# Performance work log

Hardware: AMD Instinct MI355X
Metric: run time of the kernel (lower is better)

## Reference

```python
import jax, jax.numpy as jnp
import numpy as np

# Constants from the torch module
S_DECAY = 0.95    # sentence_decay
P_DECAY = 0.99    # paragraph_decay
D_DECAY = 0.999   # document_decay
ALPHA = 0.1       # delta_update alpha for sentence/paragraph
DOC_ALPHA = 0.05  # delta_update alpha for document
BETA = 1.0
PARA_GROUP = 5    # sentences per paragraph
EPS = 1e-12       # F.normalize eps


def _normalize(x):
    # matches torch.nn.functional.normalize(x, dim=-1)
    return x / jnp.maximum(jnp.linalg.norm(x, axis=-1, keepdims=True), EPS)


def _delta_step(M, kn, v, alpha, beta):
    # M: [H, dk, dv]; kn: [dk] (already L2-normalized); v: [dv]
    # M_new = M @ (I - alpha * kn kn^T) + beta * kn v^T   (erase matrix is symmetric,
    # so the einsum 'hkv,hkj->hjv' form equals this rank-1 update -- no dk x dk matrix needed)
    kTM = jnp.einsum('k,hkv->hv', kn, M)                       # [H, dv]
    return M - alpha * kn[None, :, None] * kTM[:, None, :] \
             + beta * (kn[:, None] * v[None, :])[None, :, :]


def _scan_updates(M0, K, V, decay, alpha, beta):
    # Streaming delta-rule: per step, decay then erase/write.
    def step(M, kv):
        k, v = kv
        M = M * decay
        M = _delta_step(M, _normalize(k), v, alpha, beta)
        return M, None
    M, _ = jax.lax.scan(step, M0, (K, V))
    return M


def setup_inputs() -> dict:
    key = jax.random.key(0)
    ks = jax.random.split(key, 7)
    T, d_emb, d_k, d_v, H = 1000, 768, 256, 256, 8
    emb = jax.random.normal(ks[0], (T, d_emb), dtype=jnp.float32)
    q = jax.random.normal(ks[1], (d_k,), dtype=jnp.float32)
    W_k = jax.random.normal(ks[2], (d_emb, d_k), dtype=jnp.float32) * 0.02
    b_k = jax.random.normal(ks[3], (d_k,), dtype=jnp.float32) * 0.02
    W_v = jax.random.normal(ks[4], (d_emb, d_v), dtype=jnp.float32) * 0.02
    b_v = jax.random.normal(ks[5], (d_v,), dtype=jnp.float32) * 0.02
    M_sent0 = jnp.zeros((H, d_k, d_v), dtype=jnp.float32)
    M_para0 = jnp.zeros((H, d_k, d_v), dtype=jnp.float32)
    M_doc0 = jnp.zeros((H, d_k, d_v), dtype=jnp.float32)
    return {"emb": emb, "q": q, "W_k": W_k, "b_k": b_k, "W_v": W_v, "b_v": b_v,
            "M_sent0": M_sent0, "M_para0": M_para0, "M_doc0": M_doc0}


def reference(emb, q, W_k, b_k, W_v, b_v, M_sent0, M_para0, M_doc0):
    T, d_emb = emb.shape
    # Level 1: sentence memory -- one delta update per sentence embedding
    K = emb @ W_k + b_k            # [T, dk]
    V = emb @ W_v + b_v            # [T, dv]
    M_sent = _scan_updates(M_sent0, K, V, S_DECAY, ALPHA, BETA)
    # Level 2: paragraph memory -- mean of each group of 5 sentence embeddings
    para_emb = emb.reshape(T // PARA_GROUP, PARA_GROUP, d_emb).mean(axis=1)
    PK = para_emb @ W_k + b_k
    PV = para_emb @ W_v + b_v
    M_para = _scan_updates(M_para0, PK, PV, P_DECAY, ALPHA, BETA)
    # Level 3: document memory -- single update from paragraph-memory statistics
    doc_k = M_para.mean(axis=0).mean(axis=-1)   # [dk]
    doc_v = M_para.mean(axis=0).mean(axis=0)    # [dv]
    M_doc = M_doc0 * D_DECAY
    M_doc = _delta_step(M_doc, _normalize(doc_k), doc_v, DOC_ALPHA, BETA)
    # recall(q, level='all')
    qn = _normalize(q)
    def recall(M):
        return jnp.einsum('hkv,k->hv', M, qn).mean(axis=0)   # [dv]
    return 0.2 * recall(M_sent) + 0.3 * recall(M_para) + 0.5 * recall(M_doc)
```

## Files before the change

### kernel.cpp

```cpp
#include <hip/hip_runtime.h>
#include <hip/hip_bf16.h>

#define ALPHA   0.1f
#define S_DECAY 0.95f
#define P_DECAY 0.99f
#define D_EMB   768
#define DK      256

template<int ctrl, int row_mask>
__device__ __forceinline__ float dpp_add(float x) {
    int y = __builtin_amdgcn_update_dpp(0, __float_as_int(x), ctrl, row_mask, 0xF, true);
    return x + __int_as_float(y);
}

template<int N>
__device__ __forceinline__ void wave_allred_arr(float (&x)[N]) {
#pragma unroll
    for (int n = 0; n < N; ++n) x[n] = dpp_add<0xB1,  0xF>(x[n]);
#pragma unroll
    for (int n = 0; n < N; ++n) x[n] = dpp_add<0x4E,  0xF>(x[n]);
#pragma unroll
    for (int n = 0; n < N; ++n) x[n] = dpp_add<0x141, 0xF>(x[n]);
#pragma unroll
    for (int n = 0; n < N; ++n) x[n] = dpp_add<0x140, 0xF>(x[n]);
#pragma unroll
    for (int n = 0; n < N; ++n) x[n] = dpp_add<0x142, 0xA>(x[n]);
#pragma unroll
    for (int n = 0; n < N; ++n) x[n] = dpp_add<0x143, 0xC>(x[n]);
#pragma unroll
    for (int n = 0; n < N; ++n)
        x[n] = __int_as_float(__builtin_amdgcn_readlane(__float_as_int(x[n]), 63));
}

__device__ __forceinline__ float dot4v(const float4& a, const float4& b) {
    float t0 = a.x * b.x; t0 = fmaf(a.y, b.y, t0);
    float t1 = a.z * b.z; t1 = fmaf(a.w, b.w, t1);
    return t0 + t1;
}

__device__ __forceinline__ float rl(float x, int lane) {
    return __int_as_float(__builtin_amdgcn_readlane(__float_as_int(x), lane));
}

__global__ __launch_bounds__(256) void prep_kernel(
    const float* __restrict__ emb,
    const float* __restrict__ Wk, const float* __restrict__ bk,
    const float* __restrict__ Wv, const float* __restrict__ bv,
    float* __restrict__ K, float* __restrict__ V, float* __restrict__ USrev,
    float* __restrict__ out, int T)
{
    const int tid = threadIdx.x;
    const int bid = blockIdx.x;
    const int NBLK = (T / 4) * 2;
    if (bid >= NBLK) {
        const int PADS = ((T + 63) / 64) * 64;
        for (int i = tid; i < (PADS - T) * DK; i += 256) USrev[(size_t)T * DK + i] = 0.f;
        out[tid] = 0.f;
        return;
    }
    const int mat = bid & 1;
    const int r0  = (bid >> 1) * 4;

    __shared__ float se[4][D_EMB];
    __shared__ float s_red[4][4];

    const float4* emb4 = reinterpret_cast<const float4*>(emb);
#pragma unroll
    for (int r = 0; r < 4; ++r) {
        if (tid < D_EMB / 4)
            reinterpret_cast<float4*>(se[r])[tid] = emb4[(size_t)(r0 + r) * (D_EMB / 4) + tid];
    }
    __syncthreads();

    const float* Wp = mat ? Wv : Wk;
    const float* bp = mat ? bv : bk;
    const int j = tid;

    float a0 = 0.f, a1 = 0.f, a2 = 0.f, a3 = 0.f;
    float c0 = Wp[j],        c1 = Wp[j + DK],     c2 = Wp[j + 2*DK], c3 = Wp[j + 3*DK];
    float p0 = Wp[j + 4*DK], p1 = Wp[j + 5*DK],   p2 = Wp[j + 6*DK], p3 = Wp[j + 7*DK];

    for (int d = 0; d < D_EMB; d += 4) {
        int dn = d + 8; if (dn >= D_EMB) dn = 0;
        const float* wn = Wp + (size_t)dn * DK + j;
        float n0 = wn[0], n1 = wn[DK], n2 = wn[2*DK], n3 = wn[3*DK];

        float4 e0 = *reinterpret_cast<const float4*>(&se[0][d]);
        float4 e1 = *reinterpret_cast<const float4*>(&se[1][d]);
        float4 e2 = *reinterpret_cast<const float4*>(&se[2][d]);
        float4 e3 = *reinterpret_cast<const float4*>(&se[3][d]);
// ... 10 lines not shown
        c0 = p0; c1 = p1; c2 = p2; c3 = p3;
        p0 = n0; p1 = n1; p2 = n2; p3 = n3;
    }

    float bj = bp[j];
    float o0 = a0 + bj, o1 = a1 + bj, o2 = a2 + bj, o3 = a3 + bj;
    float* dst = mat ? V : K;
    dst[(size_t)(r0 + 0) * DK + j] = o0;
    dst[(size_t)(r0 + 1) * DK + j] = o1;
    dst[(size_t)(r0 + 2) * DK + j] = o2;
    dst[(size_t)(r0 + 3) * DK + j] = o3;

    if (mat == 0) {
        const int wave = tid >> 6, l = tid & 63;
        float red[4] = { o0*o0, o1*o1, o2*o2, o3*o3 };
        wave_allred_arr(red);
        if (l == 0) {
            s_red[wave][0] = red[0]; s_red[wave][1] = red[1];
            s_red[wave][2] = red[2]; s_red[wave][3] = red[3];
        }
        __syncthreads();
        float t0 = s_red[0][0] + s_red[1][0] + s_red[2][0] + s_red[3][0];
        float t1 = s_red[0][1] + s_red[1][1] + s_red[2][1] + s_red[3][1];
        float t2 = s_red[0][2] + s_red[1][2] + s_red[2][2] + s_red[3][2];
        float t3 = s_red[0][3] + s_red[1][3] + s_red[2][3] + s_red[3][3];
        USrev[(size_t)(T - 1 - (r0 + 0)) * DK + j] = o0 * (1.0f / fmaxf(sqrtf(t0), 1e-12f));
        USrev[(size_t)(T - 1 - (r0 + 1)) * DK + j] = o1 * (1.0f / fmaxf(sqrtf(t1), 1e-12f));
        USrev[(size_t)(T - 1 - (r0 + 2)) * DK + j] = o2 * (1.0f / fmaxf(sqrtf(t2), 1e-12f));
        USrev[(size_t)(T - 1 - (r0 + 3)) * DK + j] = o3 * (1.0f / fmaxf(sqrtf(t3), 1e-12f));
    }
}

#define SU_STRIDE 260
__global__ __launch_bounds__(512) void mid_kernel(
    const float* __restrict__ K, const float* __restrict__ V,
    const float* __restrict__ USrev,
    float* __restrict__ UPrev, float* __restrict__ UPfwd,
    float* __restrict__ PV, float* __restrict__ SVv,
    float* __restrict__ AinvT, float* __restrict__ F1, float* __restrict__ biasF,
    int P, int NCS, int NCP)
{
    __shared__ __align__(16) float sU[64 * SU_STRIDE];
    __shared__ __align__(16) float sA[64 * 65];
    __shared__ float s_pd[64];
    __shared__ float s_sv[64];
    __shared__ float4 s_f1w[4][64];
    float* sX = sU;

    const int tid = threadIdx.x, wv = tid >> 6, l = tid & 63;
    const int bid = blockIdx.x;
    int type, m;
    if (bid < NCS)            { type = 0; m = bid; }
    else if (bid < NCS + NCP) { type = 1; m = bid - NCS; }
    else                      { type = 2; m = bid - NCS - NCP; }

    if (type == 2) {
        if (tid < 64) s_pd[tid] = powf(P_DECAY, (float)tid);
        __syncthreads();
    }

    if (type == 0) {
        const float4* U4 = reinterpret_cast<const float4*>(USrev) + (size_t)m * 4096;
        for (int idx = tid; idx < 4096; idx += 512) {
            float4 t = U4[idx];
            int row = idx >> 6, c4 = (idx & 63) << 2;
            *reinterpret_cast<float4*>(&sU[row * SU_STRIDE + c4]) = t;
        }
    } else if (type == 1) {
        if (tid < 256) {
            const float4* K4 = reinterpret_cast<const float4*>(K);
            for (int ii = 0; ii < 16; ii += 2) {
                const int iA = wv * 16 + ii, iB = iA + 1;
                const int pA = P - 1 - (64 * m + iA);
                const int pB = P - 1 - (64 * m + iB);
                float4 ka[5], kb[5];
                if (pA >= 0) {
#pragma unroll
                    for (int s = 0; s < 5; ++s) ka[s] = K4[(size_t)(5 * pA + s) * 64 + l];
                }
                if (pB >= 0) {
#pragma unroll
                    for (int s = 0; s < 5; ++s) kb[s] = K4[(size_t)(5 * pB + s) * 64 + l];
                }
// ... 172 lines not shown
        float x[16];
#pragma unroll
        for (int r = 0; r < 16; ++r) x[r] = (base + r == l && wv < 4) ? 1.f : 0.f;
        for (int s = 0; s < 4; ++s) {
            if (wv == s) {
#pragma unroll
                for (int i = 1; i < 16; ++i)
#pragma unroll
                    for (int jj = 0; jj < 16; ++jj)
                        if (jj < i)
                            x[i] = fmaf(-sA[(base + i) * 65 + (base + jj)], x[jj], x[i]);
#pragma unroll
                for (int r = 0; r < 16; ++r) sX[(base + r) * 65 + l] = x[r];
            }
            __syncthreads();
            if (wv > s && wv < 4) {
#pragma unroll
                for (int i = 0; i < 16; ++i) {
                    float xi = sX[(s * 16 + i) * 65 + l];
#pragma unroll
                    for (int r = 0; r < 16; ++r)
                        x[r] = fmaf(-sA[(base + r) * 65 + (s * 16 + i)], xi, x[r]);
                }
            }
        }
    }
    __syncthreads();

    float* dstA = AinvT + (size_t)bid * 4096;
    for (int idx = tid; idx < 4096; idx += 512) {
        int jcol = idx >> 6, irow = idx & 63;
        dstA[idx] = sX[irow * 65 + jcol];
    }
}

__global__ __launch_bounds__(512) void solve_kernel(
    const float* __restrict__ USrev, const float* __restrict__ UPrev,
    const float* __restrict__ UPfwd, const float* __restrict__ AinvT,
    const float* __restrict__ F1, const float* __restrict__ biasF,
    const float* __restrict__ q,
    float* __restrict__ BS, float* __restrict__ BPB1, float* __restrict__ BPB2,
    float* __restrict__ gscal, int NCS, int NCP)
{
    __shared__ float s_cp[8][64], s_cp2[8][64];
    __shared__ float4 s_part[8][64], s_part2[8][64];
    __shared__ float s_powd[65];
    const int tid = threadIdx.x, wave = tid >> 6, l = tid & 63;
    const int wb = wave * 8;
    if (tid <= 64) s_powd[tid] = powf(P_DECAY, (float)tid);

    float4 q4 = reinterpret_cast<const float4*>(q)[l];
    float qs[1] = { dot4v(q4, q4) };
    wave_allred_arr(qs);
    float qinv = 1.0f / fmaxf(sqrtf(qs[0]), 1e-12f);
    float4 qn = make_float4(q4.x * qinv, q4.y * qinv, q4.z * qinv, q4.w * qinv);
    __syncthreads();

    if (blockIdx.x == 0) {
        float4 w1 = qn;
        const float4* U4 = reinterpret_cast<const float4*>(USrev);
        float4 curU[8]; float curX[8];
#pragma unroll
        for (int r = 0; r < 8; ++r) {
            curU[r] = U4[(size_t)(wb + r) * 64 + l];
            curX[r] = AinvT[(size_t)(wb + r) * 64 + l];
        }
        for (int m = 0; m < NCS; ++m) {
            float4 nxtU[8]; float nxtX[8];
            if (m + 1 < NCS) {
#pragma unroll
                for (int r = 0; r < 8; ++r) {
                    nxtU[r] = U4[(size_t)(m + 1) * 4096 + (size_t)(wb + r) * 64 + l];
                    nxtX[r] = AinvT[(size_t)(m + 1) * 4096 + (size_t)(wb + r) * 64 + l];
                }
            }
            float d[8];
#pragma unroll
            for (int r = 0; r < 8; ++r) d[r] = dot4v(curU[r], w1);
            wave_allred_arr(d);
            if (l == 0) {
#pragma unroll
                for (int r = 0; r < 8; ++r) BS[m * 64 + wb + r] = d[r];
            }
            float cp = 0.f;
#pragma unroll
            for (int r = 0; r < 8; ++r) cp = fmaf(curX[r], d[r], cp);
            s_cp[wave][l] = cp;
            __syncthreads();
            float cl = 0.f;
#pragma unroll
            for (int w = 0; w < 8; ++w) cl += s_cp[w][l];
            float4 part = make_float4(0.f, 0.f, 0.f, 0.f);
#pragma unroll
            for (int r = 0; r < 8; ++r) {
                float ci = rl(cl, wb + r);
                part.x = fmaf(ci, curU[r].x, part.x); part.y = fmaf(ci, curU[r].y, part.y);
                part.z = fmaf(ci, curU[r].z, part.z); part.w = fmaf(ci, curU[r].w, part.w);
            }
            s_part[wave][l] = part;
            __syncthreads();
            float4 s = make_float4(0.f, 0.f, 0.f, 0.f);
#pragma unroll
            for (int w = 0; w < 8; ++w) {
                float4 p = s_part[w][l];
                s.x += p.x; s.y += p.y; s.z += p.z; s.w += p.w;
            }
            w1.x = fmaf(-ALPHA, s.x, w1.x); w1.y = fmaf(-ALPHA, s.y, w1.y);
            w1.z = fmaf(-ALPHA, s.z, w1.z); w1.w = fmaf(-ALPHA, s.w, w1.w);
            if (m + 1 < NCS) {
#pragma unroll
                for (int r = 0; r < 8; ++r) { curU[r] = nxtU[r]; curX[r] = nxtX[r]; }
            }
        }
    } else {
        {
            float4 w1 = qn;
            float4 w2 = make_float4(1.f, 1.f, 1.f, 1.f);
            const float4* U4 = reinterpret_cast<const float4*>(UPrev);
            float4 curU[8]; float curX[8];
#pragma unroll
            for (int r = 0; r < 8; ++r) {
                curU[r] = U4[(size_t)(wb + r) * 64 + l];
                curX[r] = AinvT[(size_t)NCS * 4096 + (size_t)(wb + r) * 64 + l];
            }
            for (int m = 0; m < NCP; ++m) {
                float4 nxtU[8]; float nxtX[8];
                if (m + 1 < NCP) {
#pragma unroll
                    for (int r = 0; r < 8; ++r) {
                        nxtU[r] = U4[(size_t)(m + 1) * 4096 + (size_t)(wb + r) * 64 + l];
                        nxtX[r] = AinvT[(size_t)(NCS + m + 1) * 4096 + (size_t)(wb + r) * 64 + l];
                    }
                }
                float d[16];
#pragma unroll
                for (int r = 0; r < 8; ++r) {
                    d[r]     = dot4v(curU[r], w1);
                    d[8 + r] = dot4v(curU[r], w2);
                }
                wave_allred_arr(d);
                if (l == 0) {
#pragma unroll
                    for (int r = 0; r < 8; ++r) {
                        BPB1[m * 64 + wb + r] = d[r];
                        BPB2[m * 64 + wb + r] = d[8 + r];
                    }
                }
                float cp1 = 0.f, cp2 = 0.f;
#pragma unroll
                for (int r = 0; r < 8; ++r) {
                    cp1 = fmaf(curX[r], d[r], cp1);
                    cp2 = fmaf(curX[r], d[8 + r], cp2);
                }
                s_cp[wave][l] = cp1; s_cp2[wave][l] = cp2;
                __syncthreads();
                float cl1 = 0.f, cl2 = 0.f;
#pragma unroll
                for (int w = 0; w < 8; ++w) { cl1 += s_cp[w][l]; cl2 += s_cp2[w][l]; }
                float4 p1 = make_float4(0.f,0.f,0.f,0.f), p2 = make_float4(0.f,0.f,0.f,0.f);
#pragma unroll
                for (int r = 0; r < 8; ++r) {
                    float c1 = rl(cl1, wb + r), c2 = rl(cl2, wb + r);
                    p1.x = fmaf(c1, curU[r].x, p1.x); p1.y = fmaf(c1, curU[r].y, p1.y);
                    p1.z = fmaf(c1, curU[r].z, p1.z); p1.w = fmaf(c1, curU[r].w, p1.w);
                    p2.x = fmaf(c2, curU[r].x, p2.x); p2.y = fmaf(c2, curU[r].y, p2.y);
                    p2.z = fmaf(c2, curU[r].z, p2.z); p2.w = fmaf(c2, curU[r].w, p2.w);
                }
                s_part[wave][l] = p1; s_part2[wave][l] = p2;
                __syncthreads();
                float4 s1 = make_float4(0.f,0.f,0.f,0.f), s2 = make_float4(0.f,0.f,0.f,0.f);
#pragma unroll
                for (int w = 0; w < 8; ++w) {
                    float4 a = s_part[w][l];  float4 b = s_part2[w][l];
                    s1.x += a.x; s1.y += a.y; s1.z += a.z; s1.w += a.w;
                    s2.x += b.x; s2.y += b.y; s2.z += b.z; s2.w += b.w;
                }
                w1.x = fmaf(-ALPHA, s1.x, w1.x); w1.y = fmaf(-ALPHA, s1.y, w1.y);
                w1.z = fmaf(-ALPHA, s1.z, w1.z); w1.w = fmaf(-ALPHA, s1.w, w1.w);
                w2.x = fmaf(-ALPHA, s2.x, w2.x); w2.y = fmaf(-ALPHA, s2.y, w2.y);
                w2.z = fmaf(-ALPHA, s2.z, w2.z); w2.w = fmaf(-ALPHA, s2.w, w2.w);
                if (m + 1 < NCP) {
#pragma unroll
                    for (int r = 0; r < 8; ++r) { curU[r] = nxtU[r]; curX[r] = nxtX[r]; }
                }
            }
        }
        __syncthreads();
        float4 y = make_float4(0.f, 0.f, 0.f, 0.f);
        {
            const float4* U4 = reinterpret_cast<const float4*>(UPfwd);
            float4 curU[8]; float curX[8];
#pragma unroll
            for (int r = 0; r < 8; ++r) {
                curU[r] = U4[(size_t)(wb + r) * 64 + l];
                curX[r] = AinvT[(size_t)(NCS + NCP) * 4096 + (size_t)(wb + r) * 64 + l];
            }
            for (int m = 0; m < NCP; ++m) {
                float4 nxtU[8]; float nxtX[8];
                if (m + 1 < NCP) {
#pragma unroll
                    for (int r = 0; r < 8; ++r) {
                        nxtU[r] = U4[(size_t)(m + 1) * 4096 + (size_t)(wb + r) * 64 + l];
                        nxtX[r] = AinvT[(size_t)(NCS + NCP + m + 1) * 4096 + (size_t)(wb + r) * 64 + l];
                    }
                }
                float biasr[8];
#pragma unroll
                for (int r = 0; r < 8; ++r) biasr[r] = biasF[m * 64 + wb + r];
                float4 f1 = reinterpret_cast<const float4*>(F1)[(size_t)m * 64 + l];
                float d[8];
#pragma unroll
                for (int r = 0; r < 8; ++r) d[r] = dot4v(curU[r], y);
                wave_allred_arr(d);
#pragma unroll
                for (int r = 0; r < 8; ++r)
                    d[r] = fmaf(s_powd[wb + r + 1], d[r], biasr[r]);
                float cp = 0.f;
#pragma unroll
                for (int r = 0; r < 8; ++r) cp = fmaf(curX[r], d[r], cp);
                s_cp[wave][l] = cp;
                __syncthreads();
                float cl = 0.f;
#pragma unroll
                for (int w = 0; w < 8; ++w) cl += s_cp[w][l];
                float4 part = make_float4(0.f, 0.f, 0.f, 0.f);
#pragma unroll
                for (int r = 0; r < 8; ++r) {
                    float ci = s_powd[63 - (wb + r)] * rl(cl, wb + r);
                    part.x = fmaf(ci, curU[r].x, part.x); part.y = fmaf(ci, curU[r].y, part.y);
                    part.z = fmaf(ci, curU[r].z, part.z); part.w = fmaf(ci, curU[r].w, part.w);
                }
                s_part[wave][l] = part;
                __syncthreads();
                float4 s = make_float4(0.f, 0.f, 0.f, 0.f);
#pragma unroll
                for (int w = 0; w < 8; ++w) {
                    float4 p = s_part[w][l];
                    s.x += p.x; s.y += p.y; s.z += p.z; s.w += p.w;
                }
                float d64 = s_powd[64];
                y.x = fmaf(d64, y.x, fmaf(-ALPHA, s.x, f1.x));
                y.y = fmaf(d64, y.y, fmaf(-ALPHA, s.y, f1.y));
                y.z = fmaf(d64, y.z, fmaf(-ALPHA, s.z, f1.z));
                y.w = fmaf(d64, y.w, fmaf(-ALPHA, s.w, f1.w));
                if (m + 1 < NCP) {
#pragma unroll
                    for (int r = 0; r < 8; ++r) { curU[r] = nxtU[r]; curX[r] = nxtX[r]; }
                }
            }
        }
        float fin[2] = { dot4v(y, y), dot4v(qn, y) };
        wave_allred_arr(fin);
        if (tid == 0) gscal[0] = fin[1] / fmaxf(sqrtf(fin[0]), 2.56e-10f);
    }
}

__global__ __launch_bounds__(256) void accum_kernel(
    const float* __restrict__ V, const float* __restrict__ PV,
    const float* __restrict__ AinvT,
    const float* __restrict__ BS, const float* __restrict__ BPB1,
    const float* __restrict__ BPB2, const float* __restrict__ gscal,
    float* __restrict__ out, int T, int P, int NCS, int NCP)
{
    __shared__ float s_b[64], s_cp[4][64], wc[64];
    const int b = blockIdx.x, t = threadIdx.x;
    const float* src; const float* B; int i0, realN, chunk, ci; float decay;
    if (b < NCS)            { src = V;  B = BS;   ci = b;             realN = T; decay = S_DECAY; chunk = b; }
    else if (b < NCS + NCP) { src = PV; B = BPB1; ci = b - NCS;       realN = P; decay = P_DECAY; chunk = b; }
    else                    { src = PV; B = BPB2; ci = b - NCS - NCP; realN = P; decay = P_DECAY; chunk = b - NCP; }
    i0 = ci * 64;
    if (t < 64) s_b[t] = B[ci * 64 + t];
    __syncthreads();
    {
        const int part = t >> 6, k = t & 63;
        const float* Xc = AinvT + (size_t)chunk * 4096;
        float cp = 0.f;
#pragma unroll
        for (int jj = 0; jj < 16; ++jj) {
            int j = part * 16 + jj;
            cp = fmaf(Xc[j * 64 + k], s_b[j], cp);
        }
        s_cp[part][k] = cp;
    }
    __syncthreads();
    if (t < 64) {
        float c = s_cp[0][t] + s_cp[1][t] + s_cp[2][t] + s_cp[3][t];
        wc[t] = powf(decay, (float)(i0 + t)) * c;
    }
    __syncthreads();
    const int k = t;
    float acc = 0.f;
    for (int ii = 0; ii < 64; ++ii) {
        int i = i0 + ii;
        if (i < realN)
            acc = fmaf(wc[ii], src[(size_t)(realN - 1 - i) * DK + k], acc);
    }
    float wlev;
    if (b < NCS)            wlev = 0.2f;
    else if (b < NCS + NCP) wlev = 0.3f;
    else                    wlev = (0.5f / 256.0f) * gscal[0];
    atomicAdd(&out[k], wlev * acc);
}

extern "C" void kernel_launch(void* const* d_in, const int* in_sizes, int n_in,
                              void* d_out, int out_size, void* d_ws, size_t ws_size,
                              hipStream_t stream) {
    const float* emb = (const float*)d_in[0];
    const float* q   = (const float*)d_in[1];
    const float* Wk  = (const float*)d_in[2];
    const float* bk  = (const float*)d_in[3];
    const float* Wv  = (const float*)d_in[4];
    const float* bv  = (const float*)d_in[5];

    const int T = in_sizes[0] / D_EMB;
    const int P = T / 5;
    const int NCS  = (T + 63) / 64;
    const int NCP  = (P + 63) / 64;
    const int PADS = NCS * 64;
    const int PADP = NCP * 64;
    const int NCH  = NCS + 2 * NCP;

    float* ws    = (float*)d_ws;
    float* K     = ws;
    float* V     = K     + (size_t)T * DK;
    float* PV    = V     + (size_t)T * DK;
    float* USrev = PV    + (size_t)PADP * DK;
    float* UPrev = USrev + (size_t)PADS * DK;
    float* UPfwd = UPrev + (size_t)PADP * DK;
    float* SVv   = UPfwd + (size_t)PADP * DK;
    float* AinvT = SVv   + PADP;
    float* F1    = AinvT + (size_t)NCH * 4096;
    float* biasF = F1    + (size_t)NCP * 256;
    float* BS    = biasF + PADP;
    float* BPB1  = BS    + PADS;
    float* BPB2  = BPB1  + PADP;
    float* gscal = BPB2  + PADP;

    prep_kernel<<<(T / 4) * 2 + 1, 256, 0, stream>>>(emb, Wk, bk, Wv, bv,
                                                     K, V, USrev, (float*)d_out, T);
    mid_kernel<<<NCH, 512, 0, stream>>>(K, V, USrev, UPrev, UPfwd, PV, SVv,
                                        AinvT, F1, biasF, P, NCS, NCP);
    solve_kernel<<<2, 512, 0, stream>>>(USrev, UPrev, UPfwd, AinvT, F1, biasF, q,
                                        BS, BPB1, BPB2, gscal, NCS, NCP);
    accum_kernel<<<NCH, 256, 0, stream>>>(V, PV, AinvT, BS, BPB1, BPB2, gscal,
                                          (float*)d_out, T, P, NCS, NCP);
}
```

Measured before the change: 180.2 us.

## Fuse solve into mid kernel via last-block atomic counter

Removes the separate solve kernel launch by having the last finishing block of the chunk-preparation kernel, detected with an atomic counter and threadfence, perform the sequential recurrence solves. The counter is reset in the prep kernel. This saves a launch and the inter-kernel gap, but the sentence and paragraph solves, previously run in parallel on two blocks, are now serialized in one block, and shared memory usage grows.

```diff
diff --git a/kernel.cpp b/kernel.cpp
--- a/kernel.cpp
+++ b/kernel.cpp
@@ -47,7 +47,7 @@
     const float* __restrict__ Wk, const float* __restrict__ bk,
     const float* __restrict__ Wv, const float* __restrict__ bv,
     float* __restrict__ K, float* __restrict__ V, float* __restrict__ USrev,
-    float* __restrict__ out, int T)
+    float* __restrict__ out, int* __restrict__ counter, int T)
 {
     const int tid = threadIdx.x;
     const int bid = blockIdx.x;
@@ -56,6 +56,7 @@
         const int PADS = ((T + 63) / 64) * 64;
         for (int i = tid; i < (PADS - T) * DK; i += 256) USrev[(size_t)T * DK + i] = 0.f;
         out[tid] = 0.f;
+        if (tid == 0) counter[0] = 0;
         return;
     }
     const int mat = bid & 1;
@@ -132,12 +133,15 @@
 }
 
 #define SU_STRIDE 260
-__global__ __launch_bounds__(512) void mid_kernel(
+__global__ __launch_bounds__(512) void mega_kernel(
     const float* __restrict__ K, const float* __restrict__ V,
     const float* __restrict__ USrev,
     float* __restrict__ UPrev, float* __restrict__ UPfwd,
     float* __restrict__ PV, float* __restrict__ SVv,
     float* __restrict__ AinvT, float* __restrict__ F1, float* __restrict__ biasF,
+    const float* __restrict__ q,
+    float* __restrict__ BS, float* __restrict__ BPB1, float* __restrict__ BPB2,
+    float* __restrict__ gscal, int* __restrict__ counter,
     int P, int NCS, int NCP)
 {
     __shared__ __align__(16) float sU[64 * SU_STRIDE];
@@ -145,10 +149,15 @@
     __shared__ float s_pd[64];
     __shared__ float s_sv[64];
     __shared__ float4 s_f1w[4][64];
+    __shared__ float s_cp[8][64], s_cp2[8][64];
+    __shared__ float4 s_part[8][64], s_part2[8][64];
+    __shared__ float s_powd[65];
+    __shared__ int s_last;
     float* sX = sU;
 
     const int tid = threadIdx.x, wv = tid >> 6, l = tid & 63;
     const int bid = blockIdx.x;
+    const int NCH = NCS + 2 * NCP;
     int type, m;
     if (bid < NCS)            { type = 0; m = bid; }
     else if (bid < NCS + NCP) { type = 1; m = bid - NCS; }
@@ -387,87 +396,87 @@
         int jcol = idx >> 6, irow = idx & 63;
         dstA[idx] = sX[irow * 65 + jcol];
     }
-}
-
-__global__ __launch_bounds__(512) void solve_kernel(
-    const float* __restrict__ USrev, const float* __restrict__ UPrev,
-    const float* __restrict__ UPfwd, const float* __restrict__ AinvT,
-    const float* __restrict__ F1, const float* __restrict__ biasF,
-    const float* __restrict__ q,
-    float* __restrict__ BS, float* __restrict__ BPB1, float* __restrict__ BPB2,
-    float* __restrict__ gscal, int NCS, int NCP)
-{
-    __shared__ float s_cp[8][64], s_cp2[8][64];
-    __shared__ float4 s_part[8][64], s_part2[8][64];
-    __shared__ float s_powd[65];
-    const int tid = threadIdx.x, wave = tid >> 6, l = tid & 63;
-    const int wb = wave * 8;
-    if (tid <= 64) s_powd[tid] = powf(P_DECAY, (float)tid);
-
-    float4 q4 = reinterpret_cast<const float4*>(q)[l];
-    float qs[1] = { dot4v(q4, q4) };
-    wave_allred_arr(qs);
-    float qinv = 1.0f / fmaxf(sqrtf(qs[0]), 1e-12f);
-    float4 qn = make_float4(q4.x * qinv, q4.y * qinv, q4.z * qinv, q4.w * qinv);
-    __syncthreads();
-
-    if (blockIdx.x == 0) {
-        float4 w1 = qn;
-        const float4* U4 = reinterpret_cast<const float4*>(USrev);
-        float4 curU[8]; float curX[8];
-#pragma unroll
-        for (int r = 0; r < 8; ++r) {
-            curU[r] = U4[(size_t)(wb + r) * 64 + l];
-            curX[r] = AinvT[(size_t)(wb + r) * 64 + l];
-        }
-        for (int m = 0; m < NCS; ++m) {
-            float4 nxtU[8]; float nxtX[8];
-            if (m + 1 < NCS) {
+
+    __syncthreads();
+    if (tid == 0) {
+        __threadfence();
+        int v = atomicAdd(counter, 1);
+        s_last = (v == NCH - 1) ? 1 : 0;
+    }
+    __syncthreads();
+    if (!s_last) return;
+    __threadfence();
+
+    {
+        const int wave = wv, wb = wave * 8;
+        if (tid <= 64) s_powd[tid] = powf(P_DECAY, (float)tid);
+
+        float4 q4 = reinterpret_cast<const float4*>(q)[l];
+        float qs[1] = { dot4v(q4, q4) };
+        wave_allred_arr(qs);
+        float qinv = 1.0f / fmaxf(sqrtf(qs[0]), 1e-12f);
+        float4 qn = make_float4(q4.x * qinv, q4.y * qinv, q4.z * qinv, q4.w * qinv);
+        __syncthreads();
+
+        {
+            float4 w1 = qn;
+            const float4* U4 = reinterpret_cast<const float4*>(USrev);
+            float4 curU[8]; float curX[8];
+#pragma unroll
+            for (int r = 0; r < 8; ++r) {
+                curU[r] = U4[(size_t)(wb + r) * 64 + l];
+                curX[r] = AinvT[(size_t)(wb + r) * 64 + l];
+            }
+            for (int mm = 0; mm < NCS; ++mm) {
+                float4 nxtU[8]; float nxtX[8];
+                if (mm + 1 < NCS) {
+#pragma unroll
+                    for (int r = 0; r < 8; ++r) {
+                        nxtU[r] = U4[(size_t)(mm + 1) * 4096 + (size_t)(wb + r) * 64 + l];
+                        nxtX[r] = AinvT[(size_t)(mm + 1) * 4096 + (size_t)(wb + r) * 64 + l];
+                    }
+                }
+                float d[8];
+#pragma unroll
+                for (int r = 0; r < 8; ++r) d[r] = dot4v(curU[r], w1);
+                wave_allred_arr(d);
+                if (l == 0) {
+#pragma unroll
+                    for (int r = 0; r < 8; ++r) BS[mm * 64 + wb + r] = d[r];
+                }
+                float cp = 0.f;
+#pragma unroll
+                for (int r = 0; r < 8; ++r) cp = fmaf(curX[r], d[r], cp);
+                s_cp[wave][l] = cp;
+                __syncthreads();
+                float cl = 0.f;
+#pragma unroll
+                for (int w = 0; w < 8; ++w) cl += s_cp[w][l];
+                float4 part = make_float4(0.f, 0.f, 0.f, 0.f);
 #pragma unroll
                 for (int r = 0; r < 8; ++r) {
-                    nxtU[r] = U4[(size_t)(m + 1) * 4096 + (size_t)(wb + r) * 64 + l];
-                    nxtX[r] = AinvT[(size_t)(m + 1) * 4096 + (size_t)(wb + r) * 64 + l];
-                }
-            }
-            float d[8];
-#pragma unroll
-            for (int r = 0; r < 8; ++r) d[r] = dot4v(curU[r], w1);
-            wave_allred_arr(d);
-            if (l == 0) {
-#pragma unroll
-                for (int r = 0; r < 8; ++r) BS[m * 64 + wb + r] = d[r];
-            }
-            float cp = 0.f;
-#pragma unroll
-            for (int r = 0; r < 8; ++r) cp = fmaf(curX[r], d[r], cp);
-            s_cp[wave][l] = cp;
-            __syncthreads();
-            float cl = 0.f;
-#pragma unroll
-            for (int w = 0; w < 8; ++w) cl += s_cp[w][l];
-            float4 part = make_float4(0.f, 0.f, 0.f, 0.f);
-#pragma unroll
-            for (int r = 0; r < 8; ++r) {
-                float ci = rl(cl, wb + r);
-                part.x = fmaf(ci, curU[r].x, part.x); part.y = fmaf(ci, curU[r].y, part.y);
-                part.z = fmaf(ci, curU[r].z, part.z); part.w = fmaf(ci, curU[r].w, part.w);
-            }
-            s_part[wave][l] = part;
-            __syncthreads();
-            float4 s = make_float4(0.f, 0.f, 0.f, 0.f);
-#pragma unroll
-            for (int w = 0; w < 8; ++w) {
-                float4 p = s_part[w][l];
-                s.x += p.x; s.y += p.y; s.z += p.z; s.w += p.w;
-            }
-            w1.x = fmaf(-ALPHA, s.x, w1.x); w1.y = fmaf(-ALPHA, s.y, w1.y);
-            w1.z = fmaf(-ALPHA, s.z, w1.z); w1.w = fmaf(-ALPHA, s.w, w1.w);
-            if (m + 1 < NCS) {
-#pragma unroll
-                for (int r = 0; r < 8; ++r) { curU[r] = nxtU[r]; curX[r] = nxtX[r]; }
-            }
-        }
-    } else {
+                    float ci = rl(cl, wb + r);
+                    part.x = fmaf(ci, curU[r].x, part.x); part.y = fmaf(ci, curU[r].y, part.y);
+                    part.z = fmaf(ci, curU[r].z, part.z); part.w = fmaf(ci, curU[r].w, part.w);
+                }
+                s_part[wave][l] = part;
+                __syncthreads();
+                float4 s = make_float4(0.f, 0.f, 0.f, 0.f);
+#pragma unroll
+                for (int w = 0; w < 8; ++w) {
+                    float4 p = s_part[w][l];
+                    s.x += p.x; s.y += p.y; s.z += p.z; s.w += p.w;
+                }
+                w1.x = fmaf(-ALPHA, s.x, w1.x); w1.y = fmaf(-ALPHA, s.y, w1.y);
+                w1.z = fmaf(-ALPHA, s.z, w1.z); w1.w = fmaf(-ALPHA, s.w, w1.w);
+                if (mm + 1 < NCS) {
+#pragma unroll
+                    for (int r = 0; r < 8; ++r) { curU[r] = nxtU[r]; curX[r] = nxtX[r]; }
+                }
+            }
+        }
+        __syncthreads();
+
         {
             float4 w1 = qn;
             float4 w2 = make_float4(1.f, 1.f, 1.f, 1.f);
@@ -478,13 +487,13 @@
                 curU[r] = U4[(size_t)(wb + r) * 64 + l];
                 curX[r] = AinvT[(size_t)NCS * 4096 + (size_t)(wb + r) * 64 + l];
             }
-            for (int m = 0; m < NCP; ++m) {
+            for (int mm = 0; mm < NCP; ++mm) {
                 float4 nxtU[8]; float nxtX[8];
-                if (m + 1 < NCP) {
+                if (mm + 1 < NCP) {
 #pragma unroll
                     for (int r = 0; r < 8; ++r) {
-                        nxtU[r] = U4[(size_t)(m + 1) * 4096 + (size_t)(wb + r) * 64 + l];
-                        nxtX[r] = AinvT[(size_t)(NCS + m + 1) * 4096 + (size_t)(wb + r) * 64 + l];
+                        nxtU[r] = U4[(size_t)(mm + 1) * 4096 + (size_t)(wb + r) * 64 + l];
+                        nxtX[r] = AinvT[(size_t)(NCS + mm + 1) * 4096 + (size_t)(wb + r) * 64 + l];
                     }
                 }
                 float d[16];
@@ -497,8 +506,8 @@
                 if (l == 0) {
 #pragma unroll
                     for (int r = 0; r < 8; ++r) {
-                        BPB1[m * 64 + wb + r] = d[r];
-                        BPB2[m * 64 + wb + r] = d[8 + r];
+                        BPB1[mm * 64 + wb + r] = d[r];
+                        BPB2[mm * 64 + wb + r] = d[8 + r];
                     }
                 }
                 float cp1 = 0.f, cp2 = 0.f;
@@ -534,79 +543,79 @@
                 w1.z = fmaf(-ALPHA, s1.z, w1.z); w1.w = fmaf(-ALPHA, s1.w, w1.w);
                 w2.x = fmaf(-ALPHA, s2.x, w2.x); w2.y = fmaf(-ALPHA, s2.y, w2.y);
                 w2.z = fmaf(-ALPHA, s2.z, w2.z); w2.w = fmaf(-ALPHA, s2.w, w2.w);
-                if (m + 1 < NCP) {
+                if (mm + 1 < NCP) {
 #pragma unroll
                     for (int r = 0; r < 8; ++r) { curU[r] = nxtU[r]; curX[r] = nxtX[r]; }
                 }
             }
-        }
-        __syncthreads();
-        float4 y = make_float4(0.f, 0.f, 0.f, 0.f);
-        {
-            const float4* U4 = reinterpret_cast<const float4*>(UPfwd);
-            float4 curU[8]; float curX[8];
-#pragma unroll
-            for (int r = 0; r < 8; ++r) {
-                curU[r] = U4[(size_t)(wb + r) * 64 + l];
-                curX[r] = AinvT[(size_t)(NCS + NCP) * 4096 + (size_t)(wb + r) * 64 + l];
-            }
-            for (int m = 0; m < NCP; ++m) {
-                float4 nxtU[8]; float nxtX[8];
-                if (m + 1 < NCP) {
+            __syncthreads();
+            float4 y = make_float4(0.f, 0.f, 0.f, 0.f);
+            {
+                const float4* Uf4 = reinterpret_cast<const float4*>(UPfwd);
+                float4 cU[8]; float cX[8];
+#pragma unroll
+                for (int r = 0; r < 8; ++r) {
+                    cU[r] = Uf4[(size_t)(wb + r) * 64 + l];
+                    cX[r] = AinvT[(size_t)(NCS + NCP) * 4096 + (size_t)(wb + r) * 64 + l];
+                }
+                for (int mm = 0; mm < NCP; ++mm) {
+                    float4 nU[8]; float nX[8];
+                    if (mm + 1 < NCP) {
+#pragma unroll
+                        for (int r = 0; r < 8; ++r) {
+                            nU[r] = Uf4[(size_t)(mm + 1) * 4096 + (size_t)(wb + r) * 64 + l];
+                            nX[r] = AinvT[(size_t)(NCS + NCP + mm + 1) * 4096 + (size_t)(wb + r) * 64 + l];
+                        }
+                    }
+                    float biasr[8];
+#pragma unroll
+                    for (int r = 0; r < 8; ++r) biasr[r] = biasF[mm * 64 + wb + r];
+                    float4 f1 = reinterpret_cast<const float4*>(F1)[(size_t)mm * 64 + l];
+                    float d[8];
+#pragma unroll
+                    for (int r = 0; r < 8; ++r) d[r] = dot4v(cU[r], y);
+                    wave_allred_arr(d);
+#pragma unroll
+                    for (int r = 0; r < 8; ++r)
+                        d[r] = fmaf(s_powd[wb + r + 1], d[r], biasr[r]);
+                    float cp = 0.f;
+#pragma unroll
+                    for (int r = 0; r < 8; ++r) cp = fmaf(cX[r], d[r], cp);
+                    s_cp[wave][l] = cp;
+                    __syncthreads();
+                    float cl = 0.f;
+#pragma unroll
+                    for (int w = 0; w < 8; ++w) cl += s_cp[w][l];
+                    float4 part = make_float4(0.f, 0.f, 0.f, 0.f);
 #pragma unroll
                     for (int r = 0; r < 8; ++r) {
-                        nxtU[r] = U4[(size_t)(m + 1) * 4096 + (size_t)(wb + r) * 64 + l];
-                        nxtX[r] = AinvT[(size_t)(NCS + NCP + m + 1) * 4096 + (size_t)(wb + r) * 64 + l];
-                    }
-                }
-                float biasr[8];
-#pragma unroll
-                for (int r = 0; r < 8; ++r) biasr[r] = biasF[m * 64 + wb + r];
-                float4 f1 = reinterpret_cast<const float4*>(F1)[(size_t)m * 64 + l];
-                float d[8];
-#pragma unroll
-                for (int r = 0; r < 8; ++r) d[r] = dot4v(curU[r], y);
-                wave_allred_arr(d);
-#pragma unroll
-                for (int r = 0; r < 8; ++r)
-                    d[r] = fmaf(s_powd[wb + r + 1], d[r], biasr[r]);
-                float cp = 0.f;
-#pragma unroll
-                for (int r = 0; r < 8; ++r) cp = fmaf(curX[r], d[r], cp);
-                s_cp[wave][l] = cp;
-                __syncthreads();
-                float cl = 0.f;
-#pragma unroll
-                for (int w = 0; w < 8; ++w) cl += s_cp[w][l];
-                float4 part = make_float4(0.f, 0.f, 0.f, 0.f);
-#pragma unroll
-                for (int r = 0; r < 8; ++r) {
-                    float ci = s_powd[63 - (wb + r)] * rl(cl, wb + r);
-                    part.x = fmaf(ci, curU[r].x, part.x); part.y = fmaf(ci, curU[r].y, part.y);
-                    part.z = fmaf(ci, curU[r].z, part.z); part.w = fmaf(ci, curU[r].w, part.w);
-                }
-                s_part[wave][l] = part;
-                __syncthreads();
-                float4 s = make_float4(0.f, 0.f, 0.f, 0.f);
-#pragma unroll
-                for (int w = 0; w < 8; ++w) {
-                    float4 p = s_part[w][l];
-                    s.x += p.x; s.y += p.y; s.z += p.z; s.w += p.w;
-                }
-                float d64 = s_powd[64];
-                y.x = fmaf(d64, y.x, fmaf(-ALPHA, s.x, f1.x));
-                y.y = fmaf(d64, y.y, fmaf(-ALPHA, s.y, f1.y));
-                y.z = fmaf(d64, y.z, fmaf(-ALPHA, s.z, f1.z));
-                y.w = fmaf(d64, y.w, fmaf(-ALPHA, s.w, f1.w));
-                if (m + 1 < NCP) {
-#pragma unroll
-                    for (int r = 0; r < 8; ++r) { curU[r] = nxtU[r]; curX[r] = nxtX[r]; }
-                }
-            }
-        }
-        float fin[2] = { dot4v(y, y), dot4v(qn, y) };
-        wave_allred_arr(fin);
-        if (tid == 0) gscal[0] = fin[1] / fmaxf(sqrtf(fin[0]), 2.56e-10f);
+                        float ci = s_powd[63 - (wb + r)] * rl(cl, wb + r);
+                        part.x = fmaf(ci, cU[r].x, part.x); part.y = fmaf(ci, cU[r].y, part.y);
+                        part.z = fmaf(ci, cU[r].z, part.z); part.w = fmaf(ci, cU[r].w, part.w);
+                    }
+                    s_part[wave][l] = part;
+                    __syncthreads();
+                    float4 s = make_float4(0.f, 0.f, 0.f, 0.f);
+#pragma unroll
+                    for (int w = 0; w < 8; ++w) {
+                        float4 p = s_part[w][l];
+                        s.x += p.x; s.y += p.y; s.z += p.z; s.w += p.w;
+                    }
+                    float d64 = s_powd[64];
+                    y.x = fmaf(d64, y.x, fmaf(-ALPHA, s.x, f1.x));
+                    y.y = fmaf(d64, y.y, fmaf(-ALPHA, s.y, f1.y));
+                    y.z = fmaf(d64, y.z, fmaf(-ALPHA, s.z, f1.z));
+                    y.w = fmaf(d64, y.w, fmaf(-ALPHA, s.w, f1.w));
+                    if (mm + 1 < NCP) {
+#pragma unroll
+                        for (int r = 0; r < 8; ++r) { cU[r] = nU[r]; cX[r] = nX[r]; }
+                    }
+                }
+            }
+            float fin[2] = { dot4v(y, y), dot4v(qn, y) };
+            wave_allred_arr(fin);
+            if (tid == 0) gscal[0] = fin[1] / fmaxf(sqrtf(fin[0]), 2.56e-10f);
+        }
     }
 }
 
@@ -690,13 +699,13 @@
     float* BPB1  = BS    + PADS;
     float* BPB2  = BPB1  + PADP;
     float* gscal = BPB2  + PADP;
+    int*   counter = (int*)(gscal + 4);
 
     prep_kernel<<<(T / 4) * 2 + 1, 256, 0, stream>>>(emb, Wk, bk, Wv, bv,
-                                                     K, V, USrev, (float*)d_out, T);
-    mid_kernel<<<NCH, 512, 0, stream>>>(K, V, USrev, UPrev, UPfwd, PV, SVv,
-                                        AinvT, F1, biasF, P, NCS, NCP);
-    solve_kernel<<<2, 512, 0, stream>>>(USrev, UPrev, UPfwd, AinvT, F1, biasF, q,
-                                        BS, BPB1, BPB2, gscal, NCS, NCP);
+                                                     K, V, USrev, (float*)d_out, counter, T);
+    mega_kernel<<<NCH, 512, 0, stream>>>(K, V, USrev, UPrev, UPfwd, PV, SVv,
+                                         AinvT, F1, biasF, q,
+                                         BS, BPB1, BPB2, gscal, counter, P, NCS, NCP);
     accum_kernel<<<NCH, 256, 0, stream>>>(V, PV, AinvT, BS, BPB1, BPB2, gscal,
                                           (float*)d_out, T, P, NCS, NCP);
 }
```

New measurement: 200.3 us. +11.1%, slower.

## Fuse solve and accumulate kernels, recomputing chunk prefixes per block

Applied to the files above, without the earlier changes.

Merges the two-block sequential solve kernel into the per-chunk accumulate kernel. Each block now redoes the sequential prefix recurrence up to its own chunk and keeps the result in shared memory instead of reading it back from global buffers. This removes one kernel launch and the global round trip for BS/BPB and gscal. In exchange the prefix work is duplicated across blocks, the last block's recurrence length is unchanged, and the paragraph-forward recurrence now runs in every second-paragraph block rather than once. The next-chunk register prefetch is also gone.

```diff
diff --git a/kernel.cpp b/kernel.cpp
--- a/kernel.cpp
+++ b/kernel.cpp
@@ -389,19 +389,25 @@
     }
 }
 
-__global__ __launch_bounds__(512) void solve_kernel(
+__global__ __launch_bounds__(512) void accum2_kernel(
+    const float* __restrict__ V, const float* __restrict__ PV,
     const float* __restrict__ USrev, const float* __restrict__ UPrev,
     const float* __restrict__ UPfwd, const float* __restrict__ AinvT,
     const float* __restrict__ F1, const float* __restrict__ biasF,
     const float* __restrict__ q,
-    float* __restrict__ BS, float* __restrict__ BPB1, float* __restrict__ BPB2,
-    float* __restrict__ gscal, int NCS, int NCP)
+    float* __restrict__ out, int T, int P, int NCS, int NCP)
 {
-    __shared__ float s_cp[8][64], s_cp2[8][64];
-    __shared__ float4 s_part[8][64], s_part2[8][64];
+    __shared__ float s_cp[8][64];
+    __shared__ float4 s_part[8][64];
     __shared__ float s_powd[65];
-    const int tid = threadIdx.x, wave = tid >> 6, l = tid & 63;
-    const int wb = wave * 8;
+    __shared__ float s_b[64];
+    __shared__ float s_cpa[4][64];
+    __shared__ float wc[64];
+    __shared__ float s_gs[1];
+
+    const int b = blockIdx.x, tid = threadIdx.x;
+    const int wave = tid >> 6, l = tid & 63, wb = wave * 8;
+
     if (tid <= 64) s_powd[tid] = powf(P_DECAY, (float)tid);
 
     float4 q4 = reinterpret_cast<const float4*>(q)[l];
@@ -411,32 +417,41 @@
     float4 qn = make_float4(q4.x * qinv, q4.y * qinv, q4.z * qinv, q4.w * qinv);
     __syncthreads();
 
-    if (blockIdx.x == 0) {
-        float4 w1 = qn;
-        const float4* U4 = reinterpret_cast<const float4*>(USrev);
-        float4 curU[8]; float curX[8];
-#pragma unroll
-        for (int r = 0; r < 8; ++r) {
-            curU[r] = U4[(size_t)(wb + r) * 64 + l];
-            curX[r] = AinvT[(size_t)(wb + r) * 64 + l];
-        }
-        for (int m = 0; m < NCS; ++m) {
-            float4 nxtU[8]; float nxtX[8];
-            if (m + 1 < NCS) {
-#pragma unroll
-                for (int r = 0; r < 8; ++r) {
-                    nxtU[r] = U4[(size_t)(m + 1) * 4096 + (size_t)(wb + r) * 64 + l];
-                    nxtX[r] = AinvT[(size_t)(m + 1) * 4096 + (size_t)(wb + r) * 64 + l];
-                }
-            }
+    int ci, chunk, realN; const float* src; float decay;
+    if (b < NCS)              { ci = b;             chunk = b;        src = V;  decay = S_DECAY; realN = T; }
+    else if (b < NCS + NCP)   { ci = b - NCS;       chunk = NCS + ci; src = PV; decay = P_DECAY; realN = P; }
+    else                      { ci = b - NCS - NCP; chunk = NCS + ci; src = PV; decay = P_DECAY; realN = P; }
+
+    {
+        const float4* U4; const float* Xb; float4 w1;
+        if (b < NCS) {
+            U4 = reinterpret_cast<const float4*>(USrev); Xb = AinvT; w1 = qn;
+        } else if (b < NCS + NCP) {
+            U4 = reinterpret_cast<const float4*>(UPrev); Xb = AinvT + (size_t)NCS * 4096; w1 = qn;
+        } else {
+            U4 = reinterpret_cast<const float4*>(UPrev); Xb = AinvT + (size_t)NCS * 4096;
+            w1 = make_float4(1.f, 1.f, 1.f, 1.f);
+        }
+        for (int m = 0; m <= ci; ++m) {
+            float4 curU[8];
+#pragma unroll
+            for (int r = 0; r < 8; ++r)
+                curU[r] = U4[(size_t)m * 4096 + (size_t)(wb + r) * 64 + l];
             float d[8];
 #pragma unroll
             for (int r = 0; r < 8; ++r) d[r] = dot4v(curU[r], w1);
             wave_allred_arr(d);
-            if (l == 0) {
-#pragma unroll
-                for (int r = 0; r < 8; ++r) BS[m * 64 + wb + r] = d[r];
-            }
+            if (m == ci) {
+                if (l == 0) {
+#pragma unroll
+                    for (int r = 0; r < 8; ++r) s_b[wb + r] = d[r];
+                }
+                break;
+            }
+            float curX[8];
+#pragma unroll
+            for (int r = 0; r < 8; ++r)
+                curX[r] = Xb[(size_t)m * 4096 + (size_t)(wb + r) * 64 + l];
             float cp = 0.f;
 #pragma unroll
             for (int r = 0; r < 8; ++r) cp = fmaf(curX[r], d[r], cp);
@@ -448,9 +463,9 @@
             float4 part = make_float4(0.f, 0.f, 0.f, 0.f);
 #pragma unroll
             for (int r = 0; r < 8; ++r) {
-                float ci = rl(cl, wb + r);
-                part.x = fmaf(ci, curU[r].x, part.x); part.y = fmaf(ci, curU[r].y, part.y);
-                part.z = fmaf(ci, curU[r].z, part.z); part.w = fmaf(ci, curU[r].w, part.w);
+                float cw = rl(cl, wb + r);
+                part.x = fmaf(cw, curU[r].x, part.x); part.y = fmaf(cw, curU[r].y, part.y);
+                part.z = fmaf(cw, curU[r].z, part.z); part.w = fmaf(cw, curU[r].w, part.w);
             }
             s_part[wave][l] = part;
             __syncthreads();
@@ -462,172 +477,68 @@
             }
             w1.x = fmaf(-ALPHA, s.x, w1.x); w1.y = fmaf(-ALPHA, s.y, w1.y);
             w1.z = fmaf(-ALPHA, s.z, w1.z); w1.w = fmaf(-ALPHA, s.w, w1.w);
-            if (m + 1 < NCS) {
-#pragma unroll
-                for (int r = 0; r < 8; ++r) { curU[r] = nxtU[r]; curX[r] = nxtX[r]; }
-            }
-        }
-    } else {
-        {
-            float4 w1 = qn;
-            float4 w2 = make_float4(1.f, 1.f, 1.f, 1.f);
-            const float4* U4 = reinterpret_cast<const float4*>(UPrev);
-            float4 curU[8]; float curX[8];
+        }
+    }
+    __syncthreads();
+
+    if (b >= NCS + NCP) {
+        float4 y = make_float4(0.f, 0.f, 0.f, 0.f);
+        const float4* Uf4 = reinterpret_cast<const float4*>(UPfwd);
+        for (int mm = 0; mm < NCP; ++mm) {
+            float4 cU[8]; float cX[8];
 #pragma unroll
             for (int r = 0; r < 8; ++r) {
-                curU[r] = U4[(size_t)(wb + r) * 64 + l];
-                curX[r] = AinvT[(size_t)NCS * 4096 + (size_t)(wb + r) * 64 + l];
-            }
-            for (int m = 0; m < NCP; ++m) {
-                float4 nxtU[8]; float nxtX[8];
-                if (m + 1 < NCP) {
-#pragma unroll
-                    for (int r = 0; r < 8; ++r) {
-                        nxtU[r] = U4[(size_t)(m + 1) * 4096 + (size_t)(wb + r) * 64 + l];
-                        nxtX[r] = AinvT[(size_t)(NCS + m + 1) * 4096 + (size_t)(wb + r) * 64 + l];
-                    }
-                }
-                float d[16];
-#pragma unroll
-                for (int r = 0; r < 8; ++r) {
-                    d[r]     = dot4v(curU[r], w1);
-                    d[8 + r] = dot4v(curU[r], w2);
-                }
-                wave_allred_arr(d);
-                if (l == 0) {
-#pragma unroll
-                    for (int r = 0; r < 8; ++r) {
-                        BPB1[m * 64 + wb + r] = d[r];
-                        BPB2[m * 64 + wb + r] = d[8 + r];
-                    }
-                }
-                float cp1 = 0.f, cp2 = 0.f;
-#pragma unroll
-                for (int r = 0; r < 8; ++r) {
-                    cp1 = fmaf(curX[r], d[r], cp1);
-                    cp2 = fmaf(curX[r], d[8 + r], cp2);
-                }
-                s_cp[wave][l] = cp1; s_cp2[wave][l] = cp2;
-                __syncthreads();
-                float cl1 = 0.f, cl2 = 0.f;
-#pragma unroll
-                for (int w = 0; w < 8; ++w) { cl1 += s_cp[w][l]; cl2 += s_cp2[w][l]; }
-                float4 p1 = make_float4(0.f,0.f,0.f,0.f), p2 = make_float4(0.f,0.f,0.f,0.f);
-#pragma unroll
-                for (int r = 0; r < 8; ++r) {
-                    float c1 = rl(cl1, wb + r), c2 = rl(cl2, wb + r);
-                    p1.x = fmaf(c1, curU[r].x, p1.x); p1.y = fmaf(c1, curU[r].y, p1.y);
-                    p1.z = fmaf(c1, curU[r].z, p1.z); p1.w = fmaf(c1, curU[r].w, p1.w);
-                    p2.x = fmaf(c2, curU[r].x, p2.x); p2.y = fmaf(c2, curU[r].y, p2.y);
-                    p2.z = fmaf(c2, curU[r].z, p2.z); p2.w = fmaf(c2, curU[r].w, p2.w);
-                }
-                s_part[wave][l] = p1; s_part2[wave][l] = p2;
-                __syncthreads();
-                float4 s1 = make_float4(0.f,0.f,0.f,0.f), s2 = make_float4(0.f,0.f,0.f,0.f);
-#pragma unroll
-                for (int w = 0; w < 8; ++w) {
-                    float4 a = s_part[w][l];  float4 b = s_part2[w][l];
-                    s1.x += a.x; s1.y += a.y; s1.z += a.z; s1.w += a.w;
-                    s2.x += b.x; s2.y += b.y; s2.z += b.z; s2.w += b.w;
-                }
-                w1.x = fmaf(-ALPHA, s1.x, w1.x); w1.y = fmaf(-ALPHA, s1.y, w1.y);
-                w1.z = fmaf(-ALPHA, s1.z, w1.z); w1.w = fmaf(-ALPHA, s1.w, w1.w);
-                w2.x = fmaf(-ALPHA, s2.x, w2.x); w2.y = fmaf(-ALPHA, s2.y, w2.y);
-                w2.z = fmaf(-ALPHA, s2.z, w2.z); w2.w = fmaf(-ALPHA, s2.w, w2.w);
-                if (m + 1 < NCP) {
-#pragma unroll
-                    for (int r = 0; r < 8; ++r) { curU[r] = nxtU[r]; curX[r] = nxtX[r]; }
-                }
-            }
-        }
-        __syncthreads();
-        float4 y = make_float4(0.f, 0.f, 0.f, 0.f);
-        {
-            const float4* U4 = reinterpret_cast<const float4*>(UPfwd);
-            float4 curU[8]; float curX[8];
+                cU[r] = Uf4[(size_t)mm * 4096 + (size_t)(wb + r) * 64 + l];
+                cX[r] = AinvT[(size_t)(NCS + NCP + mm) * 4096 + (size_t)(wb + r) * 64 + l];
+            }
+            float biasr[8];
+#pragma unroll
+            for (int r = 0; r < 8; ++r) biasr[r] = biasF[mm * 64 + wb + r];
+            float4 f1 = reinterpret_cast<const float4*>(F1)[(size_t)mm * 64 + l];
+            float d[8];
+#pragma unroll
+            for (int r = 0; r < 8; ++r) d[r] = dot4v(cU[r], y);
+            wave_allred_arr(d);
+#pragma unroll
+            for (int r = 0; r < 8; ++r)
+                d[r] = fmaf(s_powd[wb + r + 1], d[r], biasr[r]);
+            float cp = 0.f;
+#pragma unroll
+            for (int r = 0; r < 8; ++r) cp = fmaf(cX[r], d[r], cp);
+            s_cp[wave][l] = cp;
+            __syncthreads();
+            float cl = 0.f;
+#pragma unroll
+            for (int w = 0; w < 8; ++w) cl += s_cp[w][l];
+            float4 part = make_float4(0.f, 0.f, 0.f, 0.f);
 #pragma unroll
             for (int r = 0; r < 8; ++r) {
-                curU[r] = U4[(size_t)(wb + r) * 64 + l];
-                curX[r] = AinvT[(size_t)(NCS + NCP) * 4096 + (size_t)(wb + r) * 64 + l];
-            }
-            for (int m = 0; m < NCP; ++m) {
-                float4 nxtU[8]; float nxtX[8];
-                if (m + 1 < NCP) {
-#pragma unroll
-                    for (int r = 0; r < 8; ++r) {
-                        nxtU[r] = U4[(size_t)(m + 1) * 4096 + (size_t)(wb + r) * 64 + l];
-                        nxtX[r] = AinvT[(size_t)(NCS + NCP + m + 1) * 4096 + (size_t)(wb + r) * 64 + l];
-                    }
-                }
-                float biasr[8];
-#pragma unroll
-                for (int r = 0; r < 8; ++r) biasr[r] = biasF[m * 64 + wb + r];
-                float4 f1 = reinterpret_cast<const float4*>(F1)[(size_t)m * 64 + l];
-                float d[8];
-#pragma unroll
-                for (int r = 0; r < 8; ++r) d[r] = dot4v(curU[r], y);
-                wave_allred_arr(d);
-#pragma unroll
-                for (int r = 0; r < 8; ++r)
-                    d[r] = fmaf(s_powd[wb + r + 1], d[r], biasr[r]);
-                float cp = 0.f;
-#pragma unroll
-                for (int r = 0; r < 8; ++r) cp = fmaf(curX[r], d[r], cp);
-                s_cp[wave][l] = cp;
-                __syncthreads();
-                float cl = 0.f;
-#pragma unroll
-                for (int w = 0; w < 8; ++w) cl += s_cp[w][l];
-                float4 part = make_float4(0.f, 0.f, 0.f, 0.f);
-#pragma unroll
-                for (int r = 0; r < 8; ++r) {
-                    float ci = s_powd[63 - (wb + r)] * rl(cl, wb + r);
-                    part.x = fmaf(ci, curU[r].x, part.x); part.y = fmaf(ci, curU[r].y, part.y);
-                    part.z = fmaf(ci, curU[r].z, part.z); part.w = fmaf(ci, curU[r].w, part.w);
-                }
-                s_part[wave][l] = part;
-                __syncthreads();
-                float4 s = make_float4(0.f, 0.f, 0.f, 0.f);
-#pragma unroll
-                for (int w = 0; w < 8; ++w) {
-                    float4 p = s_part[w][l];
-                    s.x += p.x; s.y += p.y; s.z += p.z; s.w += p.w;
-                }
-                float d64 = s_powd[64];
-                y.x = fmaf(d64, y.x, fmaf(-ALPHA, s.x, f1.x));
-                y.y = fmaf(d64, y.y, fmaf(-ALPHA, s.y, f1.y));
-                y.z = fmaf(d64, y.z, fmaf(-ALPHA, s.z, f1.z));
-                y.w = fmaf(d64, y.w, fmaf(-ALPHA, s.w, f1.w));
-                if (m + 1 < NCP) {
-#pragma unroll
-                    for (int r = 0; r < 8; ++r) { curU[r] = nxtU[r]; curX[r] = nxtX[r]; }
-                }
-            }
+                float cw = s_powd[63 - (wb + r)] * rl(cl, wb + r);
+                part.x = fmaf(cw, cU[r].x, part.x); part.y = fmaf(cw, cU[r].y, part.y);
+                part.z = fmaf(cw, cU[r].z, part.z); part.w = fmaf(cw, cU[r].w, part.w);
+            }
+            s_part[wave][l] = part;
+            __syncthreads();
+            float4 s = make_float4(0.f, 0.f, 0.f, 0.f);
+#pragma unroll
+            for (int w = 0; w < 8; ++w) {
+                float4 p = s_part[w][l];
+                s.x += p.x; s.y += p.y; s.z += p.z; s.w += p.w;
+            }
+            float d64 = s_powd[64];
+            y.x = fmaf(d64, y.x, fmaf(-ALPHA, s.x, f1.x));
+            y.y = fmaf(d64, y.y, fmaf(-ALPHA, s.y, f1.y));
+            y.z = fmaf(d64, y.z, fmaf(-ALPHA, s.z, f1.z));
+            y.w = fmaf(d64, y.w, fmaf(-ALPHA, s.w, f1.w));
         }
         float fin[2] = { dot4v(y, y), dot4v(qn, y) };
         wave_allred_arr(fin);
-        if (tid == 0) gscal[0] = fin[1] / fmaxf(sqrtf(fin[0]), 2.56e-10f);
-    }
-}
-
-__global__ __launch_bounds__(256) void accum_kernel(
-    const float* __restrict__ V, const float* __restrict__ PV,
-    const float* __restrict__ AinvT,
-    const float* __restrict__ BS, const float* __restrict__ BPB1,
-    const float* __restrict__ BPB2, const float* __restrict__ gscal,
-    float* __restrict__ out, int T, int P, int NCS, int NCP)
-{
-    __shared__ float s_b[64], s_cp[4][64], wc[64];
-    const int b = blockIdx.x, t = threadIdx.x;
-    const float* src; const float* B; int i0, realN, chunk, ci; float decay;
-    if (b < NCS)            { src = V;  B = BS;   ci = b;             realN = T; decay = S_DECAY; chunk = b; }
-    else if (b < NCS + NCP) { src = PV; B = BPB1; ci = b - NCS;       realN = P; decay = P_DECAY; chunk = b; }
-    else                    { src = PV; B = BPB2; ci = b - NCS - NCP; realN = P; decay = P_DECAY; chunk = b - NCP; }
-    i0 = ci * 64;
-    if (t < 64) s_b[t] = B[ci * 64 + t];
-    __syncthreads();
-    {
-        const int part = t >> 6, k = t & 63;
+        if (tid == 0) s_gs[0] = fin[1] / fmaxf(sqrtf(fin[0]), 2.56e-10f);
+        __syncthreads();
+    }
+
+    if (tid < 256) {
+        const int part = tid >> 6, k = tid & 63;
         const float* Xc = AinvT + (size_t)chunk * 4096;
         float cp = 0.f;
 #pragma unroll
@@ -635,26 +546,28 @@
             int j = part * 16 + jj;
             cp = fmaf(Xc[j * 64 + k], s_b[j], cp);
         }
-        s_cp[part][k] = cp;
-    }
-    __syncthreads();
-    if (t < 64) {
-        float c = s_cp[0][t] + s_cp[1][t] + s_cp[2][t] + s_cp[3][t];
-        wc[t] = powf(decay, (float)(i0 + t)) * c;
-    }
-    __syncthreads();
-    const int k = t;
-    float acc = 0.f;
-    for (int ii = 0; ii < 64; ++ii) {
-        int i = i0 + ii;
-        if (i < realN)
-            acc = fmaf(wc[ii], src[(size_t)(realN - 1 - i) * DK + k], acc);
-    }
-    float wlev;
-    if (b < NCS)            wlev = 0.2f;
-    else if (b < NCS + NCP) wlev = 0.3f;
-    else                    wlev = (0.5f / 256.0f) * gscal[0];
-    atomicAdd(&out[k], wlev * acc);
+        s_cpa[part][k] = cp;
+    }
+    __syncthreads();
+    if (tid < 64) {
+        float c = s_cpa[0][tid] + s_cpa[1][tid] + s_cpa[2][tid] + s_cpa[3][tid];
+        wc[tid] = powf(decay, (float)(ci * 64 + tid)) * c;
+    }
+    __syncthreads();
+    if (tid < 256) {
+        const int k = tid;
+        float acc = 0.f;
+        for (int ii = 0; ii < 64; ++ii) {
+            int i = ci * 64 + ii;
+            if (i < realN)
+                acc = fmaf(wc[ii], src[(size_t)(realN - 1 - i) * DK + k], acc);
+        }
+        float wlev;
+        if (b < NCS)            wlev = 0.2f;
+        else if (b < NCS + NCP) wlev = 0.3f;
+        else                    wlev = (0.5f / 256.0f) * s_gs[0];
+        atomicAdd(&out[k], wlev * acc);
+    }
 }
 
 extern "C" void kernel_launch(void* const* d_in, const int* in_sizes, int n_in,
@@ -686,17 +599,11 @@
     float* AinvT = SVv   + PADP;
     float* F1    = AinvT + (size_t)NCH * 4096;
     float* biasF = F1    + (size_t)NCP * 256;
-    float* BS    = biasF + PADP;
-    float* BPB1  = BS    + PADS;
-    float* BPB2  = BPB1  + PADP;
-    float* gscal = BPB2  + PADP;
 
     prep_kernel<<<(T / 4) * 2 + 1, 256, 0, stream>>>(emb, Wk, bk, Wv, bv,
                                                      K, V, USrev, (float*)d_out, T);
     mid_kernel<<<NCH, 512, 0, stream>>>(K, V, USrev, UPrev, UPfwd, PV, SVv,
                                         AinvT, F1, biasF, P, NCS, NCP);
-    solve_kernel<<<2, 512, 0, stream>>>(USrev, UPrev, UPfwd, AinvT, F1, biasF, q,
-                                        BS, BPB1, BPB2, gscal, NCS, NCP);
-    accum_kernel<<<NCH, 256, 0, stream>>>(V, PV, AinvT, BS, BPB1, BPB2, gscal,
-                                          (float*)d_out, T, P, NCS, NCP);
-}
+    accum2_kernel<<<NCH, 512, 0, stream>>>(V, PV, USrev, UPrev, UPfwd, AinvT,
+                                           F1, biasF, q, (float*)d_out, T, P, NCS, NCP);
+}
```

Result: faster. 173.4 us (median of 3 runs) (-3.8%).
